# Optimization experiments

Measured on AMD Instinct MI355X. Metric: run time of the kernel, lower is better.

Reference implementation:

```python
import jax, jax.numpy as jnp
import numpy as np

N, E, F_IN, C1, H1, C2, NUM_CLASSES, NUM_GRAPHS = 50000, 800000, 128, 64, 4, 128, 5, 32
NEG_SLOPE = 0.2


def gat_conv(x, W, att_src, att_dst, bias, src, dst, heads, out_ch):
    # x: [N, in], W: [in, heads*out_ch], att_*: [heads, out_ch], bias: [heads*out_ch]
    n = x.shape[0]
    h = (x @ W).reshape(n, heads, out_ch)                      # [N,H,C]
    a_src = jnp.sum(h * att_src, axis=-1)                      # [N,H]
    a_dst = jnp.sum(h * att_dst, axis=-1)                      # [N,H]
    alpha = a_src[src] + a_dst[dst]                            # [E,H]
    alpha = jax.nn.leaky_relu(alpha, NEG_SLOPE)
    # scatter-softmax over incoming edges of each dst node (every node has a self-loop)
    amax = jax.ops.segment_max(alpha, dst, num_segments=n)
    ealpha = jnp.exp(alpha - amax[dst])
    denom = jax.ops.segment_sum(ealpha, dst, num_segments=n)
    alpha = ealpha / (denom[dst] + 1e-16)                      # [E,H]
    msg = h[src] * alpha[..., None]                            # [E,H,C]
    out = jax.ops.segment_sum(msg, dst, num_segments=n)        # [N,H,C]
    return out.reshape(n, heads * out_ch) + bias


def setup_inputs() -> dict:
    key = jax.random.key(0)
    ks = jax.random.split(key, 12)
    x = jax.random.normal(ks[0], (N, F_IN), dtype=jnp.float32)
    edge_index = jax.random.randint(ks[1], (2, E), 0, N, dtype=jnp.int64)
    batch = jnp.sort(jax.random.randint(ks[2], (N,), 0, NUM_GRAPHS, dtype=jnp.int64))
    s1 = 1.0 / np.sqrt(F_IN)
    s2 = 1.0 / np.sqrt(H1 * C1)
    s3 = 1.0 / np.sqrt(C2)
    return {
        "x": x,
        "edge_index": edge_index,
        "batch": batch,
        "W1": jax.random.normal(ks[3], (F_IN, H1 * C1), dtype=jnp.float32) * s1,
        "att_src1": jax.random.normal(ks[4], (H1, C1), dtype=jnp.float32) * s1,
        "att_dst1": jax.random.normal(ks[5], (H1, C1), dtype=jnp.float32) * s1,
        "b1": jnp.zeros((H1 * C1,), dtype=jnp.float32),
        "W2": jax.random.normal(ks[6], (H1 * C1, C2), dtype=jnp.float32) * s2,
        "att_src2": jax.random.normal(ks[7], (1, C2), dtype=jnp.float32) * s2,
        "att_dst2": jax.random.normal(ks[8], (1, C2), dtype=jnp.float32) * s2,
        "b2": jnp.zeros((C2,), dtype=jnp.float32),
        "lin_w": jax.random.normal(ks[9], (C2, NUM_CLASSES), dtype=jnp.float32) * s3,
        "lin_b": jnp.zeros((NUM_CLASSES,), dtype=jnp.float32),
    }


def reference(x, edge_index, batch, W1, att_src1, att_dst1, b1, W2, att_src2, att_dst2, b2, lin_w, lin_b):
    n = x.shape[0]
    # PyG GATConv adds self-loops by default
    loops = jnp.arange(n, dtype=edge_index.dtype)
    src = jnp.concatenate([edge_index[0], loops])
    dst = jnp.concatenate([edge_index[1], loops])
    h = jax.nn.elu(gat_conv(x, W1, att_src1, att_dst1, b1, src, dst, H1, C1))
    h = jax.nn.elu(gat_conv(h, W2, att_src2, att_dst2, b2, src, dst, 1, C2))
    # global_mean_pool over graphs
    sums = jax.ops.segment_sum(h, batch, num_segments=NUM_GRAPHS)          # [G,C2]
    counts = jax.ops.segment_sum(jnp.ones((n,), h.dtype), batch, num_segments=NUM_GRAPHS)
    pooled = sums / jnp.maximum(counts, 1.0)[:, None]
    # dropout is identity in eval mode
    return pooled @ lin_w + lin_b
```

## Files before the change

### kernel.cpp

```cpp
#include <hip/hip_runtime.h>
#include <math.h>

#define NEG_SLOPE 0.2f

__device__ inline float lrelu(float x) { return x > 0.f ? x : NEG_SLOPE * x; }

typedef __attribute__((ext_vector_type(8))) _Float16 f16x8;
typedef __attribute__((ext_vector_type(4))) float f32x4;
typedef __attribute__((ext_vector_type(2))) float f32x2;
typedef __attribute__((ext_vector_type(4))) _Float16 h16x4;
typedef __attribute__((ext_vector_type(2))) _Float16 h16x2;

__global__ void convW_k(const float* __restrict__ W1, const float* __restrict__ W2,
                        _Float16* __restrict__ BT1, _Float16* __restrict__ BT2)
{
    int i = blockIdx.x * blockDim.x + threadIdx.x;
    if (i < 32768) {
        int n = i >> 7, k = i & 127;
        BT1[(size_t)n * 128 + k] = (_Float16)W1[(size_t)k * 256 + n];
    } else {
        int idx = i - 32768;
        int n = idx >> 8, k = idx & 255;
        BT2[(size_t)n * 256 + k] = (_Float16)W2[(size_t)k * 128 + n];
    }
}

template<int N, int K, int H, bool AF16>
__launch_bounds__(256)
__global__ void gemm_fused(const void* __restrict__ A, const _Float16* __restrict__ BT,
                           unsigned char* __restrict__ HB, const float* __restrict__ att_s,
                           const float* __restrict__ att_d, float* __restrict__ aS,
                           float* __restrict__ aD, int M)
{
    constexpr int ITERS = K / 32;
    constexpr int WN = N / 4;
    constexpr int NT = WN / 16;
    constexpr int NCH = (N * 4) / 256;
    __shared__ unsigned short As[64 * 40] __attribute__((aligned(16)));
    __shared__ unsigned short Bs[N * 40] __attribute__((aligned(16)));
    const int t = threadIdx.x;
    const int wave = t >> 6, lane = t & 63;
    const int quad = lane >> 4, l15 = lane & 15;
    const int rowBase = blockIdx.x * 64;

    f32x4 acc[4][NT];
#pragma unroll
    for (int mi = 0; mi < 4; ++mi)
#pragma unroll
        for (int ni = 0; ni < NT; ++ni)
            acc[mi][ni] = (f32x4){0.f, 0.f, 0.f, 0.f};

    const int ar = t >> 2;
    const int ak = (t & 3) << 3;
    const int bc = (t * NCH) >> 2;
    const int bks = (t * NCH) & 3;

    for (int it = 0; it < ITERS; ++it) {
        {
            int gr = rowBase + ar;
            f16x8 hv;
#pragma unroll
            for (int j = 0; j < 8; ++j) hv[j] = (_Float16)0.f;
            if (gr < M) {
                if constexpr (AF16) {
                    hv = *(const f16x8*)((const _Float16*)A + (size_t)gr * K + it * 32 + ak);
                } else {
                    const float* ap = (const float*)A + (size_t)gr * K + it * 32 + ak;
                    float4 v0 = *(const float4*)ap;
                    float4 v1 = *(const float4*)(ap + 4);
                    hv[0] = (_Float16)v0.x; hv[1] = (_Float16)v0.y;
                    hv[2] = (_Float16)v0.z; hv[3] = (_Float16)v0.w;
                    hv[4] = (_Float16)v1.x; hv[5] = (_Float16)v1.y;
                    hv[6] = (_Float16)v1.z; hv[7] = (_Float16)v1.w;
                }
            }
            *(f16x8*)&As[ar * 40 + ak] = hv;
        }
        {
            const _Float16* bp = BT + (size_t)bc * K + it * 32 + bks * 8;
            unsigned short* dp = &Bs[bc * 40 + bks * 8];
#pragma unroll
            for (int j = 0; j < NCH; ++j)
                *(f16x8*)(dp + j * 8) = *(const f16x8*)(bp + j * 8);
        }
        __syncthreads();
        f16x8 af[4], bfr[NT];
#pragma unroll
        for (int mi = 0; mi < 4; ++mi)
            af[mi] = *(const f16x8*)&As[(mi * 16 + l15) * 40 + quad * 8];
#pragma unroll
        for (int ni = 0; ni < NT; ++ni)
            bfr[ni] = *(const f16x8*)&Bs[(wave * WN + ni * 16 + l15) * 40 + quad * 8];
#pragma unroll
        for (int mi = 0; mi < 4; ++mi)
#pragma unroll
            for (int ni = 0; ni < NT; ++ni)
                acc[mi][ni] = __builtin_amdgcn_mfma_f32_16x16x32_f16(
                    af[mi], bfr[ni], acc[mi][ni], 0, 0, 0);
        __syncthreads();
    }
    float asv[NT], adv[NT];
#pragma unroll
    for (int ni = 0; ni < NT; ++ni) {
        int col = wave * WN + ni * 16 + l15;
        asv[ni] = att_s[col];
        adv[ni] = att_d[col];
    }
#pragma unroll
    for (int mi = 0; mi < 4; ++mi) {
#pragma unroll
        for (int r = 0; r < 4; ++r) {
            int row = rowBase + mi * 16 + quad * 4 + r;
            bool ok = row < M;
            float ss = 0.f, sd = 0.f;
#pragma unroll
            for (int ni = 0; ni < NT; ++ni) {
                float v = acc[mi][ni][r];
                ss += v * asv[ni];
                sd += v * adv[ni];
            }
#pragma unroll
            for (int ni = 0; ni < NT; ni += 2) {
                int pk = __builtin_amdgcn_cvt_pk_fp8_f32(acc[mi][ni][r],
                                                         acc[mi][ni + 1][r], 0, false);
                if (ok) {
                    HB[(size_t)row * N + wave * WN + ni * 16 + l15] =
                        (unsigned char)(pk & 0xff);
                    HB[(size_t)row * N + wave * WN + (ni + 1) * 16 + l15] =
                        (unsigned char)((pk >> 8) & 0xff);
                }
            }
#pragma unroll
            for (int off = 8; off > 0; off >>= 1) {
                ss += __shfl_xor(ss, off);
                sd += __shfl_xor(sd, off);
            }
            if (ok && l15 == 0) {
                if (H == 4) {
                    aS[row * 4 + wave] = ss;
                    aD[row * 4 + wave] = sd;
                } else {
                    atomicAdd(&aS[row], ss);
                    atomicAdd(&aD[row], sd);
                }
            }
        }
    }
}

#define BIN_EPT 32
__launch_bounds__(256)
__global__ void bcount_k(const int* __restrict__ dst, int* __restrict__ bcnt,
                         int ET, int E, int NBUCK)
{
    __shared__ int hist[1024];
    for (int i = threadIdx.x; i < NBUCK; i += 256) hist[i] = 0;
    __syncthreads();
    int e0 = blockIdx.x * (256 * BIN_EPT) + threadIdx.x;
#pragma unroll
    for (int j = 0; j < BIN_EPT; ++j) {
        int e = e0 + j * 256;
        if (e < ET) {
            int d = (e < E) ? dst[e] : (e - E);
            atomicAdd(&hist[d >> 6], 1);
        }
    }
    __syncthreads();
    for (int i = threadIdx.x; i < NBUCK; i += 256) {
        int c = hist[i];
        if (c > 0) atomicAdd(&bcnt[i], c);
    }
}

__global__ void bscan_k(const int* __restrict__ bcnt, int* __restrict__ bbase,
                        int* __restrict__ ccursor, int nb)
{
    __shared__ int sh[1024];
    int t = threadIdx.x;
    int v = (t < nb) ? bcnt[t] : 0;
    sh[t] = v;
    __syncthreads();
#pragma unroll
    for (int o = 1; o < 1024; o <<= 1) {
        int u = (t >= o) ? sh[t - o] : 0;
        __syncthreads();
        sh[t] += u;
        __syncthreads();
    }
    if (t < nb) {
        int excl = sh[t] - v;
        bbase[t] = excl;
        ccursor[t] = excl;
    }
    if (t == nb - 1) bbase[nb] = sh[t];
}

__launch_bounds__(256)
__global__ void binpass_k(const int* __restrict__ src, const int* __restrict__ dst,
                          int* __restrict__ ccursor, unsigned int* __restrict__ tmp,
                          int ET, int E, int NBUCK)
{
    __shared__ int hist[1024];
    for (int i = threadIdx.x; i < NBUCK; i += 256) hist[i] = 0;
    __syncthreads();
    int e0 = blockIdx.x * (256 * BIN_EPT) + threadIdx.x;
    unsigned int ev[BIN_EPT];
    int meta[BIN_EPT];
#pragma unroll
    for (int j = 0; j < BIN_EPT; ++j) {
        int e = e0 + j * 256;
        meta[j] = -1;
        if (e < ET) {
            int s, d;
            if (e < E) { s = src[e]; d = dst[e]; } else { s = e - E; d = s; }
            ev[j] = (unsigned int)s | ((unsigned int)d << 16);
            int b = d >> 6;
            int r = atomicAdd(&hist[b], 1);
            meta[j] = (r << 10) | b;
        }
    }
    __syncthreads();
    for (int i = threadIdx.x; i < NBUCK; i += 256) {
        int c = hist[i];
        hist[i] = (c > 0) ? atomicAdd(&ccursor[i], c) : 0;
    }
    __syncthreads();
#pragma unroll
    for (int j = 0; j < BIN_EPT; ++j) {
        if (meta[j] >= 0) {
            int b = meta[j] & 1023;
            int r = meta[j] >> 10;
            tmp[hist[b] + r] = ev[j];
        }
    }
}

__global__ void fine_k(const int* __restrict__ bbase, const unsigned int* __restrict__ tmp,
                       int* __restrict__ rowptr, unsigned short* __restrict__ esrc,
                       int Nn, int ET, int NBUCK)
{
    __shared__ int lcnt[64], lpre[64], lcur[64];
    int t = threadIdx.x;
    int b = blockIdx.x;
    int n0 = b << 6;
    int base = bbase[b];
    int end = bbase[b + 1];
    if (t < 64) lcnt[t] = 0;
    __syncthreads();
    for (int i = base + t; i < end; i += 256)
        atomicAdd(&lcnt[(tmp[i] >> 16) & 63], 1);
    __syncthreads();
    if (t < 64) lpre[t] = lcnt[t];
    __syncthreads();
#pragma unroll
    for (int o = 1; o < 64; o <<= 1) {
        int u = (t < 64 && t >= o) ? lpre[t - o] : 0;
        __syncthreads();
        if (t < 64) lpre[t] += u;
        __syncthreads();
    }
    if (t < 64) {
        int n = n0 + t;
        int excl = lpre[t] - lcnt[t];
        if (n < Nn) {
            rowptr[n] = base + excl;
            lcur[t] = base + excl;
        }
    }
    if (b == NBUCK - 1 && t == 0) rowptr[Nn] = ET;
    __syncthreads();
    for (int i = base + t; i < end; i += 256) {
        unsigned int v = tmp[i];
        int pos = atomicAdd(&lcur[(v >> 16) & 63], 1);
        esrc[pos] = (unsigned short)(v & 0xffffu);
    }
}

__global__ void gather1_k(const int* __restrict__ rp, const unsigned short* __restrict__ esrc,
                          const unsigned char* __restrict__ hb, const float* __restrict__ aS,
                          const float* __restrict__ aD, const float* __restrict__ bias,
                          _Float16* __restrict__ out, int Nn)
{
    int d = blockIdx.x * 4 + (threadIdx.x >> 6);
    int lane = threadIdx.x & 63;
    if (d >= Nn) return;
    int c4 = lane << 2;
    int head = lane >> 4;
    int p0 = __builtin_amdgcn_readfirstlane(rp[d]);
    int p1 = __builtin_amdgcn_readfirstlane(rp[d + 1]);
    float adh = aD[d * 4 + head];
    const float* aSh = aS + head;
    float den = 0.f;
    float ax = 0.f, ay = 0.f, az = 0.f, aw = 0.f;
    int p = p0;
    for (; p + 8 <= p1; p += 8) {
        int s[8];
#pragma unroll
        for (int j = 0; j < 8; ++j) s[j] = __builtin_amdgcn_readfirstlane(esrc[p + j]);
        unsigned int v[8];
#pragma unroll
        for (int j = 0; j < 8; ++j)
            v[j] = *(const unsigned int*)&hb[(size_t)s[j] * 256 + c4];
        float w[8];
#pragma unroll
        for (int j = 0; j < 8; ++j) w[j] = __expf(lrelu(aSh[s[j] * 4] + adh));
#pragma unroll
        for (int j = 0; j < 8; ++j) {
            den += w[j];
            f32x2 lo = __builtin_amdgcn_cvt_pk_f32_fp8((int)v[j], false);
            f32x2 hi = __builtin_amdgcn_cvt_pk_f32_fp8((int)v[j], true);
            ax += lo[0] * w[j];
            ay += lo[1] * w[j];
            az += hi[0] * w[j];
            aw += hi[1] * w[j];
        }
    }
    int rem = p1 - p;
    if (rem > 0) {
        int s[8];
        unsigned int v[8];
        float w[8];
#pragma unroll
        for (int j = 0; j < 8; ++j)
            if (j < rem) s[j] = __builtin_amdgcn_readfirstlane(esrc[p + j]);
#pragma unroll
        for (int j = 0; j < 8; ++j)
            if (j < rem) v[j] = *(const unsigned int*)&hb[(size_t)s[j] * 256 + c4];
#pragma unroll
        for (int j = 0; j < 8; ++j)
            if (j < rem) w[j] = __expf(lrelu(aSh[s[j] * 4] + adh));
#pragma unroll
        for (int j = 0; j < 8; ++j) {
            if (j < rem) {
                den += w[j];
                f32x2 lo = __builtin_amdgcn_cvt_pk_f32_fp8((int)v[j], false);
                f32x2 hi = __builtin_amdgcn_cvt_pk_f32_fp8((int)v[j], true);
                ax += lo[0] * w[j];
                ay += lo[1] * w[j];
                az += hi[0] * w[j];
                aw += hi[1] * w[j];
            }
        }
    }
    float inv = 1.f / (den + 1e-16f);
    float4 b4 = *(const float4*)&bias[c4];
    float rx, ry, rz, rw;
    rx = ax * inv + b4.x; rx = rx > 0.f ? rx : expm1f(rx);
    ry = ay * inv + b4.y; ry = ry > 0.f ? ry : expm1f(ry);
    rz = az * inv + b4.z; rz = rz > 0.f ? rz : expm1f(rz);
    rw = aw * inv + b4.w; rw = rw > 0.f ? rw : expm1f(rw);
    h16x4 r16;
    r16[0] = (_Float16)rx; r16[1] = (_Float16)ry;
    r16[2] = (_Float16)rz; r16[3] = (_Float16)rw;
    *(h16x4*)&out[(size_t)d * 256 + c4] = r16;
}

__global__ void gather2_k(const int* __restrict__ rp, const unsigned short* __restrict__ esrc,
                          const unsigned char* __restrict__ hb, const float* __restrict__ aS,
                          const float* __restrict__ aD, _Float16* __restrict__ out, int Nn)
{
    int d = blockIdx.x * 4 + (threadIdx.x >> 6);
    int lane = threadIdx.x & 63;
    if (d >= Nn) return;
    int c2 = lane << 1;
    int p0 = __builtin_amdgcn_readfirstlane(rp[d]);
    int p1 = __builtin_amdgcn_readfirstlane(rp[d + 1]);
    float adh = aD[d];
    float den = 0.f;
    float ax = 0.f, ay = 0.f;
    int p = p0;
    for (; p + 8 <= p1; p += 8) {
        int s[8];
#pragma unroll
        for (int j = 0; j < 8; ++j) s[j] = __builtin_amdgcn_readfirstlane(esrc[p + j]);
        unsigned short v[8];
#pragma unroll
        for (int j = 0; j < 8; ++j)
            v[j] = *(const unsigned short*)&hb[(size_t)s[j] * 128 + c2];
        float w[8];
#pragma unroll
        for (int j = 0; j < 8; ++j) w[j] = __expf(lrelu(aS[s[j]] + adh));
#pragma unroll
        for (int j = 0; j < 8; ++j) {
            den += w[j];
            f32x2 lo = __builtin_amdgcn_cvt_pk_f32_fp8((int)v[j], false);
            ax += lo[0] * w[j];
            ay += lo[1] * w[j];
        }
    }
    int rem = p1 - p;
    if (rem > 0) {
        int s[8];
        unsigned short v[8];
        float w[8];
#pragma unroll
        for (int j = 0; j < 8; ++j)
            if (j < rem) s[j] = __builtin_amdgcn_readfirstlane(esrc[p + j]);
#pragma unroll
        for (int j = 0; j < 8; ++j)
            if (j < rem) v[j] = *(const unsigned short*)&hb[(size_t)s[j] * 128 + c2];
#pragma unroll
        for (int j = 0; j < 8; ++j)
            if (j < rem) w[j] = __expf(lrelu(aS[s[j]] + adh));
#pragma unroll
        for (int j = 0; j < 8; ++j) {
            if (j < rem) {
                den += w[j];
                f32x2 lo = __builtin_amdgcn_cvt_pk_f32_fp8((int)v[j], false);
                ax += lo[0] * w[j];
                ay += lo[1] * w[j];
            }
        }
    }
    float inv = 1.f / (den + 1e-16f);
    h16x2 r16;
    r16[0] = (_Float16)(ax * inv);
    r16[1] = (_Float16)(ay * inv);
    *(h16x2*)&out[(size_t)d * 128 + c2] = r16;
}

__global__ void pool_k(const _Float16* __restrict__ o2, const float* __restrict__ b2,
                       const int* __restrict__ batch, float* __restrict__ sums, int Nn, int C)
{
    int c = threadIdx.x;
    int n0 = blockIdx.x * 64;
    int n1 = min(n0 + 64, Nn);
    float local = 0.f;
    int gcur = batch[n0];
    float bc = b2[c];
    for (int n = n0; n < n1; ++n) {
        int g = batch[n];
        if (g != gcur) {
            atomicAdd(&sums[gcur * C + c], local);
            local = 0.f;
            gcur = g;
        }
        float v = (float)o2[(size_t)n * C + c] + bc;
        local += v > 0.f ? v : expm1f(v);
    }
    atomicAdd(&sums[gcur * C + c], local);
}

__global__ void final_k(const float* __restrict__ sums, const int* __restrict__ batch,
                        const float* __restrict__ lin_w, const float* __restrict__ lin_b,
                        float* __restrict__ out, int Nn, int G, int C, int NC)
{
    __shared__ float inv[64];
    int t = threadIdx.x;
    if (t < G) {
        int lo = 0, hi = Nn;
        while (lo < hi) { int mid = (lo + hi) >> 1; if (batch[mid] < t) lo = mid + 1; else hi = mid; }
        int lb = lo;
        lo = 0; hi = Nn;
        while (lo < hi) { int mid = (lo + hi) >> 1; if (batch[mid] < t + 1) lo = mid + 1; else hi = mid; }
        int cnt = lo - lb;
        inv[t] = 1.f / fmaxf((float)cnt, 1.f);
    }
    __syncthreads();
    if (t < G * NC) {
        int g = t / NC, k = t % NC;
        float acc = 0.f;
        for (int c = 0; c < C; ++c) acc += sums[g * C + c] * lin_w[c * NC + k];
        out[t] = acc * inv[g] + lin_b[k];
    }
}

extern "C" void kernel_launch(void* const* d_in, const int* in_sizes, int n_in,
                              void* d_out, int out_size, void* d_ws, size_t ws_size,
                              hipStream_t stream)
{
    const float* x      = (const float*)d_in[0];
    const int*   eidx   = (const int*)d_in[1];
    const int*   batch  = (const int*)d_in[2];
    const float* W1     = (const float*)d_in[3];
    const float* att_s1 = (const float*)d_in[4];
    const float* att_d1 = (const float*)d_in[5];
    const float* b1     = (const float*)d_in[6];
    const float* W2     = (const float*)d_in[7];
    const float* att_s2 = (const float*)d_in[8];
    const float* att_d2 = (const float*)d_in[9];
    const float* b2     = (const float*)d_in[10];
    const float* lin_w  = (const float*)d_in[11];
    const float* lin_b  = (const float*)d_in[12];

    const int Nn  = in_sizes[2];
    const int E   = in_sizes[1] / 2;
    const int H1_ = 4, C1_ = 64, C2_ = 128, G = 32, NC = 5;
    const int D1 = H1_ * C1_;
    const int ET = E + Nn;
    const int NBUCK = (Nn + 63) >> 6;

    const int* srcp = eidx;
    const int* dstp = eidx + E;

    float* ws = (float*)d_ws;
    size_t off = 0;
    auto alloc = [&](size_t n) { float* p = ws + off; off += n; return p; };
    _Float16* o1h = (_Float16*)alloc((size_t)Nn * D1 / 2);
    _Float16* o2h = (_Float16*)alloc((size_t)Nn * C2_ / 2);
    float* aS1  = alloc((size_t)Nn * H1_);
    float* aD1  = alloc((size_t)Nn * H1_);
    float* aS2  = alloc(Nn);
    float* aD2  = alloc(Nn);
    float* sums = alloc((size_t)G * C2_);
    _Float16* BT1 = (_Float16*)alloc(D1 * 128 / 2);
    _Float16* BT2 = (_Float16*)alloc(C2_ * 256 / 2);
    unsigned char* hb1 = (unsigned char*)alloc((size_t)Nn * D1 / 4);
    unsigned char* hb2 = (unsigned char*)alloc((size_t)Nn * C2_ / 4);
    int* iws    = (int*)(ws + off);
    int* rowptr = iws;
    int* bcnt   = iws + Nn + 1;
    int* bbase  = iws + Nn + 1 + 1024;
    int* ccursor= iws + Nn + 1 + 2049;
    unsigned int* tmp = (unsigned int*)(iws + Nn + 1 + 2049 + 1024);
    unsigned short* esrc = (unsigned short*)(tmp + ET);

    const int GB = (Nn + 63) / 64;
    const int NW = (Nn + 3) / 4;
    const int BINB = (ET + 256 * BIN_EPT - 1) / (256 * BIN_EPT);

    hipMemsetAsync(bcnt, 0, 1024 * 4, stream);
    hipMemsetAsync(aS2, 0, (size_t)2 * Nn * 4, stream);
    bcount_k<<<BINB, 256, 0, stream>>>(dstp, bcnt, ET, E, NBUCK);
    bscan_k<<<1, 1024, 0, stream>>>(bcnt, bbase, ccursor, NBUCK);
    binpass_k<<<BINB, 256, 0, stream>>>(srcp, dstp, ccursor, tmp, ET, E, NBUCK);
    fine_k<<<NBUCK, 256, 0, stream>>>(bbase, tmp, rowptr, esrc, Nn, ET, NBUCK);

    convW_k<<<256, 256, 0, stream>>>(W1, W2, BT1, BT2);

    gemm_fused<256, 128, 4, false><<<GB, 256, 0, stream>>>(x, BT1, hb1, att_s1, att_d1,
                                                           aS1, aD1, Nn);
    gather1_k<<<NW, 256, 0, stream>>>(rowptr, esrc, hb1, aS1, aD1, b1, o1h, Nn);

    gemm_fused<128, 256, 1, true><<<GB, 256, 0, stream>>>(o1h, BT2, hb2, att_s2, att_d2,
                                                          aS2, aD2, Nn);
    gather2_k<<<NW, 256, 0, stream>>>(rowptr, esrc, hb2, aS2, aD2, o2h, Nn);

    hipMemsetAsync(sums, 0, (size_t)G * C2_ * 4, stream);
    pool_k<<<GB, C2_, 0, stream>>>(o2h, b2, batch, sums, Nn, C2_);
    final_k<<<1, 256, 0, stream>>>(sums, batch, lin_w, lin_b, (float*)d_out, Nn, G, C2_, NC);
}
```

Baseline: 324.5 us.

## Fuse mean-pool into second gather and replace attention-score atomics with LDS reduction

The second GAT gather now applies bias and ELU and accumulates per-graph sums directly through a block-level LDS reduction and atomics. This removes the o2h intermediate write/read and the separate pool kernel launch. The H=1 GEMM now reduces per-row attention scores across waves in shared memory and writes them once, instead of using global atomics. That also drops the aS2/aD2 memset. The cost is roughly one atomic per channel per block of 4 nodes into the small sums array, which may contend more than the old 64-node pool blocks.

```diff
diff --git a/kernel.cpp b/kernel.cpp
--- a/kernel.cpp
+++ b/kernel.cpp
@@ -9,7 +9,6 @@
 typedef __attribute__((ext_vector_type(4))) float f32x4;
 typedef __attribute__((ext_vector_type(2))) float f32x2;
 typedef __attribute__((ext_vector_type(4))) _Float16 h16x4;
-typedef __attribute__((ext_vector_type(2))) _Float16 h16x2;
 
 __global__ void convW_k(const float* __restrict__ W1, const float* __restrict__ W2,
                         _Float16* __restrict__ BT1, _Float16* __restrict__ BT2)
@@ -38,6 +37,7 @@
     constexpr int NCH = (N * 4) / 256;
     __shared__ unsigned short As[64 * 40] __attribute__((aligned(16)));
     __shared__ unsigned short Bs[N * 40] __attribute__((aligned(16)));
+    __shared__ float sred[2][4][64];
     const int t = threadIdx.x;
     const int wave = t >> 6, lane = t & 63;
     const int quad = lane >> 4, l15 = lane & 15;
@@ -135,14 +135,26 @@
                 ss += __shfl_xor(ss, off);
                 sd += __shfl_xor(sd, off);
             }
-            if (ok && l15 == 0) {
+            if (l15 == 0) {
                 if (H == 4) {
-                    aS[row * 4 + wave] = ss;
-                    aD[row * 4 + wave] = sd;
+                    if (ok) {
+                        aS[row * 4 + wave] = ss;
+                        aD[row * 4 + wave] = sd;
+                    }
                 } else {
-                    atomicAdd(&aS[row], ss);
-                    atomicAdd(&aD[row], sd);
+                    sred[0][wave][mi * 16 + quad * 4 + r] = ss;
+                    sred[1][wave][mi * 16 + quad * 4 + r] = sd;
                 }
+            }
+        }
+    }
+    if (H == 1) {
+        __syncthreads();
+        if (t < 64) {
+            int row = rowBase + t;
+            if (row < M) {
+                aS[row] = sred[0][0][t] + sred[0][1][t] + sred[0][2][t] + sred[0][3][t];
+                aD[row] = sred[1][0][t] + sred[1][1][t] + sred[1][2][t] + sred[1][3][t];
             }
         }
     }
@@ -357,88 +369,94 @@
 
 __global__ void gather2_k(const int* __restrict__ rp, const unsigned short* __restrict__ esrc,
                           const unsigned char* __restrict__ hb, const float* __restrict__ aS,
-                          const float* __restrict__ aD, _Float16* __restrict__ out, int Nn)
-{
-    int d = blockIdx.x * 4 + (threadIdx.x >> 6);
+                          const float* __restrict__ aD, const float* __restrict__ b2,
+                          const int* __restrict__ batch, float* __restrict__ sums, int Nn)
+{
+    __shared__ float pv[4][128];
+    __shared__ int pg[4];
+    int wave = threadIdx.x >> 6;
+    int d = blockIdx.x * 4 + wave;
     int lane = threadIdx.x & 63;
-    if (d >= Nn) return;
     int c2 = lane << 1;
-    int p0 = __builtin_amdgcn_readfirstlane(rp[d]);
-    int p1 = __builtin_amdgcn_readfirstlane(rp[d + 1]);
-    float adh = aD[d];
-    float den = 0.f;
-    float ax = 0.f, ay = 0.f;
-    int p = p0;
-    for (; p + 8 <= p1; p += 8) {
-        int s[8];
-#pragma unroll
-        for (int j = 0; j < 8; ++j) s[j] = __builtin_amdgcn_readfirstlane(esrc[p + j]);
-        unsigned short v[8];
-#pragma unroll
-        for (int j = 0; j < 8; ++j)
-            v[j] = *(const unsigned short*)&hb[(size_t)s[j] * 128 + c2];
-        float w[8];
-#pragma unroll
-        for (int j = 0; j < 8; ++j) w[j] = __expf(lrelu(aS[s[j]] + adh));
-#pragma unroll
-        for (int j = 0; j < 8; ++j) {
-            den += w[j];
-            f32x2 lo = __builtin_amdgcn_cvt_pk_f32_fp8((int)v[j], false);
-            ax += lo[0] * w[j];
-            ay += lo[1] * w[j];
-        }
-    }
-    int rem = p1 - p;
-    if (rem > 0) {
-        int s[8];
-        unsigned short v[8];
-        float w[8];
-#pragma unroll
-        for (int j = 0; j < 8; ++j)
-            if (j < rem) s[j] = __builtin_amdgcn_readfirstlane(esrc[p + j]);
-#pragma unroll
-        for (int j = 0; j < 8; ++j)
-            if (j < rem) v[j] = *(const unsigned short*)&hb[(size_t)s[j] * 128 + c2];
-#pragma unroll
-        for (int j = 0; j < 8; ++j)
-            if (j < rem) w[j] = __expf(lrelu(aS[s[j]] + adh));
-#pragma unroll
-        for (int j = 0; j < 8; ++j) {
-            if (j < rem) {
+    bool valid = d < Nn;
+    if (lane == 0) pg[wave] = valid ? batch[d] : -1;
+    if (valid) {
+        int p0 = __builtin_amdgcn_readfirstlane(rp[d]);
+        int p1 = __builtin_amdgcn_readfirstlane(rp[d + 1]);
+        float adh = aD[d];
+        float den = 0.f;
+        float ax = 0.f, ay = 0.f;
+        int p = p0;
+        for (; p + 8 <= p1; p += 8) {
+            int s[8];
+#pragma unroll
+            for (int j = 0; j < 8; ++j) s[j] = __builtin_amdgcn_readfirstlane(esrc[p + j]);
+            unsigned short v[8];
+#pragma unroll
+            for (int j = 0; j < 8; ++j)
+                v[j] = *(const unsigned short*)&hb[(size_t)s[j] * 128 + c2];
+            float w[8];
+#pragma unroll
+            for (int j = 0; j < 8; ++j) w[j] = __expf(lrelu(aS[s[j]] + adh));
+#pragma unroll
+            for (int j = 0; j < 8; ++j) {
                 den += w[j];
                 f32x2 lo = __builtin_amdgcn_cvt_pk_f32_fp8((int)v[j], false);
                 ax += lo[0] * w[j];
                 ay += lo[1] * w[j];
             }
         }
-    }
-    float inv = 1.f / (den + 1e-16f);
-    h16x2 r16;
-    r16[0] = (_Float16)(ax * inv);
-    r16[1] = (_Float16)(ay * inv);
-    *(h16x2*)&out[(size_t)d * 128 + c2] = r16;
-}
-
-__global__ void pool_k(const _Float16* __restrict__ o2, const float* __restrict__ b2,
-                       const int* __restrict__ batch, float* __restrict__ sums, int Nn, int C)
-{
-    int c = threadIdx.x;
-    int n0 = blockIdx.x * 64;
-    int n1 = min(n0 + 64, Nn);
-    float local = 0.f;
-    int gcur = batch[n0];
-    float bc = b2[c];
-    for (int n = n0; n < n1; ++n) {
-        int g = batch[n];
-        if (g != gcur) {
-            atomicAdd(&sums[gcur * C + c], local);
-            local = 0.f;
-            gcur = g;
-        }
-        float v = (float)o2[(size_t)n * C + c] + bc;
-        local += v > 0.f ? v : expm1f(v);
-    }
-    atomicAdd(&sums[gcur * C + c], local);
+        int rem = p1 - p;
+        if (rem > 0) {
+            int s[8];
+            unsigned short v[8];
+            float w[8];
+#pragma unroll
+            for (int j = 0; j < 8; ++j)
+                if (j < rem) s[j] = __builtin_amdgcn_readfirstlane(esrc[p + j]);
+#pragma unroll
+            for (int j = 0; j < 8; ++j)
+                if (j < rem) v[j] = *(const unsigned short*)&hb[(size_t)s[j] * 128 + c2];
+#pragma unroll
+            for (int j = 0; j < 8; ++j)
+                if (j < rem) w[j] = __expf(lrelu(aS[s[j]] + adh));
+#pragma unroll
+            for (int j = 0; j < 8; ++j) {
+                if (j < rem) {
+                    den += w[j];
+                    f32x2 lo = __builtin_amdgcn_cvt_pk_f32_fp8((int)v[j], false);
+                    ax += lo[0] * w[j];
+                    ay += lo[1] * w[j];
+                }
+            }
+        }
+        float inv = 1.f / (den + 1e-16f);
+        float2 bb = *(const float2*)&b2[c2];
+        float v0 = ax * inv + bb.x; v0 = v0 > 0.f ? v0 : expm1f(v0);
+        float v1 = ay * inv + bb.y; v1 = v1 > 0.f ? v1 : expm1f(v1);
+        pv[wave][c2] = v0;
+        pv[wave][c2 + 1] = v1;
+    }
+    __syncthreads();
+    if (threadIdx.x < 128) {
+        int c = threadIdx.x;
+        float acc = 0.f;
+        int g = -1;
+#pragma unroll
+        for (int w = 0; w < 4; ++w) {
+            int gw = pg[w];
+            if (gw < 0) continue;
+            float vw = pv[w][c];
+            if (gw == g) {
+                acc += vw;
+            } else {
+                if (g >= 0) atomicAdd(&sums[g * 128 + c], acc);
+                g = gw;
+                acc = vw;
+            }
+        }
+        if (g >= 0) atomicAdd(&sums[g * 128 + c], acc);
+    }
 }
 
 __global__ void final_k(const float* __restrict__ sums, const int* __restrict__ batch,
@@ -497,7 +515,6 @@
     size_t off = 0;
     auto alloc = [&](size_t n) { float* p = ws + off; off += n; return p; };
     _Float16* o1h = (_Float16*)alloc((size_t)Nn * D1 / 2);
-    _Float16* o2h = (_Float16*)alloc((size_t)Nn * C2_ / 2);
     float* aS1  = alloc((size_t)Nn * H1_);
     float* aD1  = alloc((size_t)Nn * H1_);
     float* aS2  = alloc(Nn);
@@ -520,7 +537,7 @@
     const int BINB = (ET + 256 * BIN_EPT - 1) / (256 * BIN_EPT);
 
     hipMemsetAsync(bcnt, 0, 1024 * 4, stream);
-    hipMemsetAsync(aS2, 0, (size_t)2 * Nn * 4, stream);
+    hipMemsetAsync(sums, 0, (size_t)G * C2_ * 4, stream);
     bcount_k<<<BINB, 256, 0, stream>>>(dstp, bcnt, ET, E, NBUCK);
     bscan_k<<<1, 1024, 0, stream>>>(bcnt, bbase, ccursor, NBUCK);
     binpass_k<<<BINB, 256, 0, stream>>>(srcp, dstp, ccursor, tmp, ET, E, NBUCK);
@@ -534,9 +551,7 @@
 
     gemm_fused<128, 256, 1, true><<<GB, 256, 0, stream>>>(o1h, BT2, hb2, att_s2, att_d2,
                                                           aS2, aD2, Nn);
-    gather2_k<<<NW, 256, 0, stream>>>(rowptr, esrc, hb2, aS2, aD2, o2h, Nn);
-
-    hipMemsetAsync(sums, 0, (size_t)G * C2_ * 4, stream);
-    pool_k<<<GB, C2_, 0, stream>>>(o2h, b2, batch, sums, Nn, C2_);
+    gather2_k<<<NW, 256, 0, stream>>>(rowptr, esrc, hb2, aS2, aD2, b2, batch, sums, Nn);
+
     final_k<<<1, 256, 0, stream>>>(sums, batch, lin_w, lin_b, (float*)d_out, Nn, G, C2_, NC);
 }
```

New measurement: 325.3 us. About the same (+0.2%).
